# Optimization experiments

Measured on AMD Instinct MI355X. Metric: run time of the kernel, lower is better.

The kernel has to match this reference:

```python
import jax, jax.numpy as jnp
import numpy as np

N = 20000          # nodes
E = 320000         # edges (avg degree 16)
D_IN, D1, D2, D_OUT = 256, 512, 256, 64
EPS = 1e-5


def _glorot(key, shape):
    lim = (6.0 / (shape[0] + shape[1])) ** 0.5
    return jax.random.uniform(key, shape, jnp.float32, -lim, lim)


def setup_inputs() -> dict:
    key = jax.random.key(0)
    ks = jax.random.split(key, 8)
    x = jax.random.normal(ks[0], (N, D_IN), jnp.float32)
    edge_index = jax.random.randint(ks[1], (2, E), 0, N, dtype=jnp.int64)
    return {
        "x": x,
        "edge_index": edge_index,
        # SAGEConv 1 (SoftmaxAggregation temperature t1 over inp_dim channels)
        "t1": jnp.ones((1, D_IN), jnp.float32),
        "Wl1": _glorot(ks[2], (D_IN, D1)), "bl1": jnp.zeros((D1,), jnp.float32),
        "Wr1": _glorot(ks[3], (D_IN, D1)),
        "g1": jnp.ones((D1,), jnp.float32), "beta1": jnp.zeros((D1,), jnp.float32),
        # SAGEConv 2
        "t2": jnp.ones((1, D1), jnp.float32),
        "Wl2": _glorot(ks[4], (D1, D2)), "bl2": jnp.zeros((D2,), jnp.float32),
        "Wr2": _glorot(ks[5], (D1, D2)),
        "g2": jnp.ones((D2,), jnp.float32), "beta2": jnp.zeros((D2,), jnp.float32),
        # final linear + LayerNorm
        "Wf": _glorot(ks[6], (D2, D_OUT)), "bf": jnp.zeros((D_OUT,), jnp.float32),
        "gx": jnp.ones((D_OUT,), jnp.float32), "betax": jnp.zeros((D_OUT,), jnp.float32),
    }


def _sage_softmax(x, src, dst, t, Wl, bl, Wr, n):
    """SAGEConv with learnable per-channel SoftmaxAggregation."""
    m = x[src]                                              # [E, C] gathered messages
    a = m * t                                               # scaled logits
    amax = jax.ops.segment_max(a, dst, num_segments=n)      # [N, C]
    e = jnp.exp(a - amax[dst])
    denom = jax.ops.segment_sum(e, dst, num_segments=n)     # [N, C]
    w = e / denom[dst]                                      # segment softmax weights
    agg = jax.ops.segment_sum(m * w, dst, num_segments=n)   # weighted neighbor sum
    return agg @ Wl + bl + x @ Wr


def _graph_ln(x, g, b):
    # PyG LayerNorm mode='graph', batch=None: normalize over ALL nodes & channels
    mu = x.mean()
    std = jnp.sqrt(((x - mu) ** 2).mean())
    return (x - mu) / (std + EPS) * g + b


def _ln(x, g, b):
    mu = x.mean(-1, keepdims=True)
    var = ((x - mu) ** 2).mean(-1, keepdims=True)
    return (x - mu) / jnp.sqrt(var + EPS) * g + b


def reference(x, edge_index, t1, Wl1, bl1, Wr1, g1, beta1,
              t2, Wl2, bl2, Wr2, g2, beta2, Wf, bf, gx, betax):
    src, dst = edge_index[0], edge_index[1]
    h = _sage_softmax(x, src, dst, t1, Wl1, bl1, Wr1, N)
    h = jax.nn.relu(_graph_ln(h, g1, beta1))
    h = _sage_softmax(h, src, dst, t2, Wl2, bl2, Wr2, N)
    h = jax.nn.relu(_graph_ln(h, g2, beta2))
    p = h.mean(0, keepdims=True)                            # global_mean_pool, batch=None -> [1, 256]
    out = _ln(p @ Wf + bf, gx, betax)
    return jax.nn.relu(out)
```

## Files before the change

### kernel.cpp

```cpp
#include <hip/hip_runtime.h>
#include <math.h>

#define NODES 20000
#define MPAD  20096
#define EDGES 320000
#define EPSV  1e-5f
#define LOG2E 1.4426950408889634f

#define PREP_CNT   1250
#define PREP_CAST  5000
#define PREP_TR    512
#define PREP_TOTAL (PREP_CNT + PREP_CAST + PREP_TR + 1)

typedef short bf16x8 __attribute__((ext_vector_type(8)));
typedef float f32x4  __attribute__((ext_vector_type(4)));
typedef float f2     __attribute__((ext_vector_type(2)));

__device__ __forceinline__ unsigned short f2bf(float f) {
    unsigned int u = __float_as_uint(f);
    u = (u + 0x7fffu + ((u >> 16) & 1u)) >> 16;
    return (unsigned short)u;
}
__device__ __forceinline__ float bf2f(unsigned short h) {
    return __uint_as_float(((unsigned int)h) << 16);
}

__device__ __forceinline__ void load_lds16(const unsigned short* g, unsigned short* l) {
    __builtin_amdgcn_global_load_lds(
        (const __attribute__((address_space(1))) unsigned int*)g,
        (__attribute__((address_space(3))) unsigned int*)l, 16, 0, 0);
}

__global__ void k_prep(const int* __restrict__ dst, int* __restrict__ counts,
                       const float* __restrict__ x, unsigned short* __restrict__ xb,
                       const float* __restrict__ Wl1, const float* __restrict__ Wr1,
                       const float* __restrict__ Wl2, const float* __restrict__ Wr2,
                       unsigned short* __restrict__ o1l, unsigned short* __restrict__ o1r,
                       unsigned short* __restrict__ o2l, unsigned short* __restrict__ o2r,
                       float* __restrict__ acc, float* __restrict__ colsum) {
    int b = blockIdx.x;
    int t = threadIdx.x;
    if (b < PREP_CNT) {
        int e = b * 256 + t;
        if (e < EDGES) atomicAdd(&counts[dst[e]], 1);
    } else if (b < PREP_CNT + PREP_CAST) {
        int i = ((b - PREP_CNT) * 256 + t) * 4;
        float4 v = *(const float4*)(x + i);
        xb[i + 0] = f2bf(v.x); xb[i + 1] = f2bf(v.y);
        xb[i + 2] = f2bf(v.z); xb[i + 3] = f2bf(v.w);
    } else if (b < PREP_CNT + PREP_CAST + PREP_TR) {
        __shared__ float tile[32][33];
        int zz = b - PREP_CNT - PREP_CAST;
        int z = zz >> 7;
        int idx = zz & 127;
        const float* W = (z == 0) ? Wl1 : (z == 1) ? Wr1 : (z == 2) ? Wl2 : Wr2;
        unsigned short* Wt = (z == 0) ? o1l : (z == 1) ? o1r : (z == 2) ? o2l : o2r;
        int K = (z < 2) ? 256 : 512, N = (z < 2) ? 512 : 256;
        int nb = N / 32;
        int n0 = (idx % nb) * 32, k0 = (idx / nb) * 32;
        int tx = t & 31, ty = t >> 5;
#pragma unroll
        for (int j = 0; j < 4; j++)
            tile[ty + j * 8][tx] = W[(size_t)(k0 + ty + j * 8) * N + n0 + tx];
        __syncthreads();
#pragma unroll
        for (int j = 0; j < 4; j++)
            Wt[(size_t)(n0 + ty + j * 8) * K + k0 + tx] = f2bf(tile[tx][ty + j * 8]);
    } else {
        if (t < 4) acc[t] = 0.f;
        colsum[t] = 0.f;
    }
}

#define SCAN_B 32

__global__ void k_scan1(const int* __restrict__ counts, int* __restrict__ bsum) {
    __shared__ int sm[256];
    int t = threadIdx.x, b = blockIdx.x;
    int i0 = (b * 256 + t) * 3;
    int s = 0;
#pragma unroll
    for (int j = 0; j < 3; j++) { int i = i0 + j; if (i < NODES) s += counts[i]; }
    sm[t] = s;
    __syncthreads();
    int v = s;
#pragma unroll
    for (int o = 1; o < 256; o <<= 1) {
        int add = (t >= o) ? sm[t - o] : 0;
        __syncthreads();
        v += add;
        sm[t] = v;
        __syncthreads();
    }
    if (t == 255) bsum[b] = v;
}

__global__ void k_scan2(int* __restrict__ bsum, int* __restrict__ offs) {
    int t = threadIdx.x;
    int v = (t < SCAN_B) ? bsum[t] : 0;
    int x = v;
#pragma unroll
    for (int o = 1; o < 64; o <<= 1) {
        int y = __shfl_up(x, o);
        if (t >= o) x += y;
    }
    if (t < SCAN_B) bsum[t] = x - v;
    if (t == SCAN_B - 1) offs[NODES] = x;
}

__global__ void k_scan3(const int* __restrict__ counts, const int* __restrict__ bsum,
                        int* __restrict__ offs) {
    __shared__ int sm[256];
    int t = threadIdx.x, b = blockIdx.x;
    int i0 = (b * 256 + t) * 3;
    int c[3]; int s = 0;
#pragma unroll
    for (int j = 0; j < 3; j++) {
        int i = i0 + j;
        c[j] = (i < NODES) ? counts[i] : 0;
        s += c[j];
    }
    sm[t] = s;
    __syncthreads();
    int v = s;
#pragma unroll
    for (int o = 1; o < 256; o <<= 1) {
        int add = (t >= o) ? sm[t - o] : 0;
        __syncthreads();
        v += add;
        sm[t] = v;
        __syncthreads();
    }
    int run = bsum[b] + (v - s);
#pragma unroll
    for (int j = 0; j < 3; j++) {
        int i = i0 + j;
        if (i < NODES) { offs[i] = run; run += c[j]; }
    }
}

__global__ void k_scatter(const int* __restrict__ src, const int* __restrict__ dst,
                          const int* __restrict__ offs, int* __restrict__ cursor,
                          int* __restrict__ csr_src) {
    int e = blockIdx.x * blockDim.x + threadIdx.x;
    if (e < EDGES) {
        int d = dst[e];
        int pos = atomicAdd(&cursor[d], 1);
        csr_src[offs[d] + pos] = src[e];
    }
}

template <int C, int S, int UNR>
__global__ void k_agg(const unsigned short* __restrict__ xb, const float* __restrict__ tt,
                      const int* __restrict__ offs, const int* __restrict__ csr,
                      unsigned short* __restrict__ out) {
    constexpr int CS  = C / S;
    constexpr int VPL = CS / 64;
    constexpr int W   = VPL / 2;
    typedef unsigned int uv __attribute__((ext_vector_type(W)));
    typedef unsigned short usv __attribute__((ext_vector_type(VPL)));
    int waveg = (int)((blockIdx.x * (unsigned)blockDim.x + threadIdx.x) >> 6);
    int lane = threadIdx.x & 63;
    int node = waveg / S;
    int slice = waveg % S;
    if (node >= NODES) return;
    int beg = __builtin_amdgcn_readfirstlane(offs[node]);
    int end = __builtin_amdgcn_readfirstlane(offs[node + 1]);
    int cb = slice * CS + lane * VPL;
    const unsigned short* __restrict__ xcb = xb + cb;
    f2 tl[W], l[W], s[W];
#pragma unroll
    for (int i = 0; i < W; i++) {
        tl[i][0] = tt[cb + 2 * i] * LOG2E;
        tl[i][1] = tt[cb + 2 * i + 1] * LOG2E;
        l[i][0] = 0.f; l[i][1] = 0.f;
        s[i][0] = 0.f; s[i][1] = 0.f;
    }
    int k = beg;
    for (; k + UNR <= end; k += UNR) {
        uv v[UNR];
#pragma unroll
        for (int u = 0; u < UNR; u++) {
            int sn = csr[k + u];
            v[u] = *(const uv*)(xcb + (size_t)sn * C);
        }
#pragma unroll
        for (int u = 0; u < UNR; u++)
#pragma unroll
            for (int i = 0; i < W; i++) {
                unsigned wd = v[u][i];
                f2 xv;
                xv[0] = __uint_as_float(wd << 16);
                xv[1] = __uint_as_float(wd & 0xffff0000u);
                f2 a = xv * tl[i];
                f2 p;
                p[0] = __builtin_amdgcn_exp2f(a[0]);
                p[1] = __builtin_amdgcn_exp2f(a[1]);
                l[i] += p;
                s[i] = __builtin_elementwise_fma(p, xv, s[i]);
            }
    }
    for (; k < end; k++) {
        int sn = csr[k];
        uv vv = *(const uv*)(xcb + (size_t)sn * C);
#pragma unroll
        for (int i = 0; i < W; i++) {
            unsigned wd = vv[i];
            f2 xv;
            xv[0] = __uint_as_float(wd << 16);
            xv[1] = __uint_as_float(wd & 0xffff0000u);
            f2 a = xv * tl[i];
            f2 p;
            p[0] = __builtin_amdgcn_exp2f(a[0]);
            p[1] = __builtin_amdgcn_exp2f(a[1]);
            l[i] += p;
            s[i] = __builtin_elementwise_fma(p, xv, s[i]);
        }
    }
    bool has = end > beg;
    usv o;
#pragma unroll
    for (int i = 0; i < W; i++) {
        o[2 * i]     = f2bf(has ? s[i][0] / l[i][0] : 0.f);
        o[2 * i + 1] = f2bf(has ? s[i][1] / l[i][1] : 0.f);
    }
    *(usv*)(out + (size_t)node * C + cb) = o;
}

template <int K, int NT, int NTILES, int TN>
__global__ __launch_bounds__(256) void k_gemm_mfma(
    const unsigned short* __restrict__ A1, const unsigned short* __restrict__ B1t,
    const unsigned short* __restrict__ A2, const unsigned short* __restrict__ B2t,
    const float* __restrict__ bias, unsigned short* __restrict__ Co, int M,
    float* __restrict__ stat) {
    constexpr int NF = TN / 32;
    __shared__ short As[4 * 128 * 32];
    __shared__ short Bs[4 * TN * 32];
    __shared__ float rs[8], rq[8];

    int bx = blockIdx.x;
    int xid = bx & 7, q = bx >> 3;
    int n = q % NTILES, mh = q / NTILES;
    int m = mh * 8 + xid;
    if (m * 128 >= MPAD) return;
    int m0 = m * 128, n0 = n * TN;

    int t = threadIdx.x;
    int wv = t >> 6, lane = t & 63;
    int wm = wv & 1, wn = wv >> 1;
    int lm = lane & 15, quad = lane >> 4;
    int sr = t >> 2;
    int sc8 = (t & 3) * 8;

    f32x4 acc[4][NF] = {};

    for (int ph = 0; ph < 2; ph++) {
        const unsigned short* __restrict__ A  = ph ? A2 : A1;
        const unsigned short* __restrict__ Bt = ph ? B2t : B1t;
        for (int ks = 0; ks < K; ks += 128) {
#pragma unroll
            for (int c = 0; c < 4; c++) {
#pragma unroll
                for (int it = 0; it < 2; it++)
                    load_lds16(A + (size_t)(m0 + it * 64 + sr) * K + ks + c * 32 + sc8,
                               (unsigned short*)&As[c * 4096 + it * 2048 + wv * 512]);
#pragma unroll
                for (int it = 0; it < TN / 64; it++)
                    load_lds16(Bt + (size_t)(n0 + it * 64 + sr) * K + ks + c * 32 + sc8,
                               (unsigned short*)&Bs[c * (TN * 32) + it * 2048 + wv * 512]);
            }
            __syncthreads();
#pragma unroll
            for (int c = 0; c < 4; c++) {
                bf16x8 af[4], bfr[NF];
#pragma unroll
                for (int i = 0; i < 4; i++)
                    af[i] = *(const bf16x8*)&As[c * 4096 + (wm * 64 + i * 16 + lm) * 32 + quad * 8];
#pragma unroll
                for (int j = 0; j < NF; j++)
                    bfr[j] = *(const bf16x8*)&Bs[c * (TN * 32) + (wn * (TN / 2) + j * 16 + lm) * 32 + quad * 8];
#pragma unroll
                for (int mi = 0; mi < 4; mi++)
#pragma unroll
                    for (int nj = 0; nj < NF; nj++)
                        acc[mi][nj] = __builtin_amdgcn_mfma_f32_16x16x32_bf16(
                            af[mi], bfr[nj], acc[mi][nj], 0, 0, 0);
            }
            __syncthreads();
        }
    }

    float sum = 0.f, ss = 0.f;
#pragma unroll
    for (int mi = 0; mi < 4; mi++) {
        int rb = m0 + wm * 64 + mi * 16 + quad * 4;
#pragma unroll
        for (int nj = 0; nj < NF; nj++) {
            int col = n0 + wn * (TN / 2) + nj * 16 + lm;
            float bb = bias[col];
#pragma unroll
            for (int rg = 0; rg < 4; rg++) {
                int row = rb + rg;
                if (row < M) {
                    float y = acc[mi][nj][rg] + bb;
                    Co[(size_t)row * NT + col] = f2bf(y);
                    sum += y; ss += y * y;
                }
            }
        }
    }
#pragma unroll
    for (int o = 32; o > 0; o >>= 1) {
        sum += __shfl_xor(sum, o);
        ss  += __shfl_xor(ss, o);
    }
    if (lane == 0) { rs[wv] = sum; rq[wv] = ss; }
    __syncthreads();
    if (t == 0) {
        float a0 = 0.f, a1 = 0.f;
#pragma unroll
        for (int i = 0; i < 4; i++) { a0 += rs[i] + rs[i + 4]; a1 += rq[i] + rq[i + 4]; }
        atomicAdd(&stat[0], a0); atomicAdd(&stat[1], a1);
    }
}

template <int C>
__global__ void k_ln_relu_b(unsigned short* __restrict__ h, int n,
                            const float* __restrict__ st,
                            const float* __restrict__ g, const float* __restrict__ b) {
    typedef unsigned short us8 __attribute__((ext_vector_type(8)));
    float mu = st[0] / (float)n;
    float var = st[1] / (float)n - mu * mu;
    var = var < 0.f ? 0.f : var;
    float inv = 1.0f / (sqrtf(var) + EPSV);
    int i8 = (blockIdx.x * blockDim.x + threadIdx.x) * 8;
    if (i8 >= n) return;
    int c = i8 & (C - 1);
    us8 v = *(const us8*)(h + i8);
    us8 o;
#pragma unroll
    for (int j = 0; j < 8; j++) {
        float y = (bf2f(v[j]) - mu) * inv * g[c + j] + b[c + j];
        o[j] = f2bf(fmaxf(y, 0.f));
    }
    *(us8*)(h + i8) = o;
}

__global__ void k_ln_colsum(const unsigned short* __restrict__ h, int n,
                            const float* __restrict__ st,
                            const float* __restrict__ g, const float* __restrict__ b,
                            float* __restrict__ colsum) {
    float mu = st[0] / (float)n;
    float var = st[1] / (float)n - mu * mu;
    var = var < 0.f ? 0.f : var;
    float inv = 1.0f / (sqrtf(var) + EPSV);
    int t = threadIdx.x;
    float gv = g[t], bv = b[t];
    float local = 0.f;
    int stride = gridDim.x * blockDim.x;
    for (int i = blockIdx.x * blockDim.x + t; i < n; i += stride) {
        float y = (bf2f(h[i]) - mu) * inv * gv + bv;
        local += fmaxf(y, 0.f);
    }
    atomicAdd(&colsum[t], local);
}

__global__ void k_final(const float* __restrict__ colsum, const float* __restrict__ Wf,
                        const float* __restrict__ bf, const float* __restrict__ gx,
                        const float* __restrict__ bx, float* __restrict__ out) {
    __shared__ float p[256];
    __shared__ float red[4][64];
    int t = threadIdx.x;
    p[t] = colsum[t] * (1.0f / (float)NODES);
    __syncthreads();
    int kg = t >> 6, o = t & 63;
    float a = 0.f;
#pragma unroll
    for (int j = 0; j < 64; j++) {
        int c = kg + j * 4;
        a = fmaf(p[c], Wf[c * 64 + o], a);
    }
    red[kg][o] = a;
    __syncthreads();
    if (t < 64) {
        float acc = bf[t] + red[0][t] + red[1][t] + red[2][t] + red[3][t];
        float sum = acc;
        for (int w = 32; w > 0; w >>= 1) sum += __shfl_xor(sum, w);
        float mu = sum * (1.0f / 64.0f);
        float d = acc - mu;
        float vs = d * d;
        for (int w = 32; w > 0; w >>= 1) vs += __shfl_xor(vs, w);
        float var = vs * (1.0f / 64.0f);
        float y = d * rsqrtf(var + EPSV) * gx[t] + bx[t];
        out[t] = fmaxf(y, 0.f);
    }
}

extern "C" void kernel_launch(void* const* d_in, const int* in_sizes, int n_in,
                              void* d_out, int out_size, void* d_ws, size_t ws_size,
                              hipStream_t stream) {
    const float* x   = (const float*)d_in[0];
    const int*   ei  = (const int*)d_in[1];
    const float* t1  = (const float*)d_in[2];
    const float* Wl1 = (const float*)d_in[3];
    const float* bl1 = (const float*)d_in[4];
    const float* Wr1 = (const float*)d_in[5];
    const float* g1  = (const float*)d_in[6];
    const float* be1 = (const float*)d_in[7];
    const float* t2  = (const float*)d_in[8];
    const float* Wl2 = (const float*)d_in[9];
    const float* bl2 = (const float*)d_in[10];
    const float* Wr2 = (const float*)d_in[11];
    const float* g2  = (const float*)d_in[12];
    const float* be2 = (const float*)d_in[13];
    const float* Wf  = (const float*)d_in[14];
    const float* bf  = (const float*)d_in[15];
    const float* gx  = (const float*)d_in[16];
    const float* bx  = (const float*)d_in[17];
    float* out = (float*)d_out;

    char* ws = (char*)d_ws;
    size_t off = 0;
    auto alloc = [&](size_t bytes) { size_t o = off; off = (off + bytes + 511) & ~511ull; return o; };
    size_t o_counts = alloc((size_t)NODES * 4);
    size_t o_cursor = alloc((size_t)NODES * 4);
    size_t zero_bytes = off;
    size_t o_acc    = alloc(4 * 4);
    size_t o_colsum = alloc(256 * 4);
    size_t o_bsum = alloc((size_t)SCAN_B * 4);
    size_t o_offs = alloc((size_t)(NODES + 1) * 4);
    size_t o_csrc = alloc((size_t)EDGES * 4);
    size_t o_w1l  = alloc((size_t)512 * 256 * 2);
    size_t o_w1r  = alloc((size_t)512 * 256 * 2);
    size_t o_w2l  = alloc((size_t)256 * 512 * 2);
    size_t o_w2r  = alloc((size_t)256 * 512 * 2);
    size_t o_bufX = alloc((size_t)MPAD * 256 * 2);
    size_t o_agg  = alloc((size_t)MPAD * 512 * 2);
    size_t o_h1   = alloc((size_t)(MPAD + 512) * 512 * 2);

    int*   counts = (int*)(ws + o_counts);
    int*   cursor = (int*)(ws + o_cursor);
    float* acc    = (float*)(ws + o_acc);
    float* colsum = (float*)(ws + o_colsum);
    int*   bsum   = (int*)(ws + o_bsum);
    int*   offs   = (int*)(ws + o_offs);
    int*   csrc   = (int*)(ws + o_csrc);
    unsigned short* w1lt = (unsigned short*)(ws + o_w1l);
    unsigned short* w1rt = (unsigned short*)(ws + o_w1r);
    unsigned short* w2lt = (unsigned short*)(ws + o_w2l);
    unsigned short* w2rt = (unsigned short*)(ws + o_w2r);
    unsigned short* xb   = (unsigned short*)(ws + o_bufX);
    unsigned short* h2p  = (unsigned short*)(ws + o_bufX);
    unsigned short* aggb = (unsigned short*)(ws + o_agg);
    unsigned short* h1   = (unsigned short*)(ws + o_h1);

    const int* src = ei;
    const int* dst = ei + EDGES;

    hipMemsetAsync(ws, 0, zero_bytes, stream);

    k_prep<<<PREP_TOTAL, 256, 0, stream>>>(dst, counts, x, xb,
                                           Wl1, Wr1, Wl2, Wr2,
                                           w1lt, w1rt, w2lt, w2rt,
                                           acc, colsum);
    k_scan1<<<SCAN_B, 256, 0, stream>>>(counts, bsum);
    k_scan2<<<1, 64, 0, stream>>>(bsum, offs);
    k_scan3<<<SCAN_B, 256, 0, stream>>>(counts, bsum, offs);
    k_scatter<<<(EDGES + 255) / 256, 256, 0, stream>>>(src, dst, offs, cursor, csrc);

    k_agg<256, 2, 8><<<(NODES * 2 + 3) / 4, 256, 0, stream>>>(xb, t1, offs, csrc, aggb);
    k_gemm_mfma<256, 512, 4, 128><<<8 * 4 * 20, 256, 0, stream>>>(
        aggb, w1lt, xb, w1rt, bl1, h1, NODES, acc);
    k_ln_relu_b<512><<<NODES * 512 / 8 / 256, 256, 0, stream>>>(h1, NODES * 512, acc, g1, be1);

    k_agg<512, 2, 4><<<(NODES * 2 + 3) / 4, 256, 0, stream>>>(h1, t2, offs, csrc, aggb);
    k_gemm_mfma<512, 256, 2, 128><<<8 * 2 * 20, 256, 0, stream>>>(
        aggb, w2lt, h1, w2rt, bl2, h2p, NODES, acc + 2);

    k_ln_colsum<<<1024, 256, 0, stream>>>(h2p, NODES * 256, acc + 2, g2, be2, colsum);
    k_final<<<1, 256, 0, stream>>>(colsum, Wf, bf, gx, bx, out);
}
```

Measured before the change: 320.8 us.

## Prefetch GEMM K-slabs into registers to overlap global loads with MFMA

Replaces the direct global-to-LDS loads of 128-wide K chunks with a register-staged software pipeline over 64-wide K slabs. The next slab is loaded into registers while the MFMAs for the current slab run, then written to LDS after a barrier. This halves LDS usage, which may raise occupancy, and hides global load latency. The cost is extra VGPRs for staging, extra LDS store instructions, and more barriers per K step.

```diff
diff --git a/kernel.cpp b/kernel.cpp
--- a/kernel.cpp
+++ b/kernel.cpp
@@ -23,12 +23,6 @@
 }
 __device__ __forceinline__ float bf2f(unsigned short h) {
     return __uint_as_float(((unsigned int)h) << 16);
-}
-
-__device__ __forceinline__ void load_lds16(const unsigned short* g, unsigned short* l) {
-    __builtin_amdgcn_global_load_lds(
-        (const __attribute__((address_space(1))) unsigned int*)g,
-        (__attribute__((address_space(3))) unsigned int*)l, 16, 0, 0);
 }
 
 __global__ void k_prep(const int* __restrict__ dst, int* __restrict__ counts,
@@ -233,9 +227,12 @@
     const unsigned short* __restrict__ A2, const unsigned short* __restrict__ B2t,
     const float* __restrict__ bias, unsigned short* __restrict__ Co, int M,
     float* __restrict__ stat) {
-    constexpr int NF = TN / 32;
-    __shared__ short As[4 * 128 * 32];
-    __shared__ short Bs[4 * TN * 32];
+    constexpr int NF  = TN / 32;
+    constexpr int BIT = TN / 64;
+    constexpr int HS  = K / 64;
+    constexpr int NS  = 2 * HS;
+    __shared__ short As[2 * 128 * 32];
+    __shared__ short Bs[2 * TN * 32];
     __shared__ float rs[8], rq[8];
 
     int bx = blockIdx.x;
@@ -253,40 +250,53 @@
     int sc8 = (t & 3) * 8;
 
     f32x4 acc[4][NF] = {};
-
-    for (int ph = 0; ph < 2; ph++) {
-        const unsigned short* __restrict__ A  = ph ? A2 : A1;
-        const unsigned short* __restrict__ Bt = ph ? B2t : B1t;
-        for (int ks = 0; ks < K; ks += 128) {
-#pragma unroll
-            for (int c = 0; c < 4; c++) {
-#pragma unroll
-                for (int it = 0; it < 2; it++)
-                    load_lds16(A + (size_t)(m0 + it * 64 + sr) * K + ks + c * 32 + sc8,
-                               (unsigned short*)&As[c * 4096 + it * 2048 + wv * 512]);
-#pragma unroll
-                for (int it = 0; it < TN / 64; it++)
-                    load_lds16(Bt + (size_t)(n0 + it * 64 + sr) * K + ks + c * 32 + sc8,
-                               (unsigned short*)&Bs[c * (TN * 32) + it * 2048 + wv * 512]);
-            }
-            __syncthreads();
-#pragma unroll
-            for (int c = 0; c < 4; c++) {
-                bf16x8 af[4], bfr[NF];
-#pragma unroll
-                for (int i = 0; i < 4; i++)
-                    af[i] = *(const bf16x8*)&As[c * 4096 + (wm * 64 + i * 16 + lm) * 32 + quad * 8];
-#pragma unroll
-                for (int j = 0; j < NF; j++)
-                    bfr[j] = *(const bf16x8*)&Bs[c * (TN * 32) + (wn * (TN / 2) + j * 16 + lm) * 32 + quad * 8];
-#pragma unroll
-                for (int mi = 0; mi < 4; mi++)
-#pragma unroll
-                    for (int nj = 0; nj < NF; nj++)
-                        acc[mi][nj] = __builtin_amdgcn_mfma_f32_16x16x32_bf16(
-                            af[mi], bfr[nj], acc[mi][nj], 0, 0, 0);
-            }
-            __syncthreads();
+    bf16x8 rA[2][2];
+    bf16x8 rB[2][BIT];
+
+    auto loadslab = [&](int s) {
+        const unsigned short* __restrict__ A  = (s < HS) ? A1 : A2;
+        const unsigned short* __restrict__ Bt = (s < HS) ? B1t : B2t;
+        int kk = (s & (HS - 1)) * 64;
+#pragma unroll
+        for (int c = 0; c < 2; c++) {
+#pragma unroll
+            for (int it = 0; it < 2; it++)
+                rA[c][it] = *(const bf16x8*)(A + (size_t)(m0 + it * 64 + sr) * K + kk + c * 32 + sc8);
+#pragma unroll
+            for (int it = 0; it < BIT; it++)
+                rB[c][it] = *(const bf16x8*)(Bt + (size_t)(n0 + it * 64 + sr) * K + kk + c * 32 + sc8);
+        }
+    };
+
+    loadslab(0);
+    for (int s = 0; s < NS; s++) {
+        if (s) __syncthreads();
+#pragma unroll
+        for (int c = 0; c < 2; c++) {
+#pragma unroll
+            for (int it = 0; it < 2; it++)
+                *(bf16x8*)&As[c * 4096 + it * 2048 + t * 8] = rA[c][it];
+#pragma unroll
+            for (int it = 0; it < BIT; it++)
+                *(bf16x8*)&Bs[c * (TN * 32) + it * 2048 + t * 8] = rB[c][it];
+        }
+        __syncthreads();
+        if (s + 1 < NS) loadslab(s + 1);
+#pragma unroll
+        for (int c = 0; c < 2; c++) {
+            bf16x8 af[4], bfr[NF];
+#pragma unroll
+            for (int i = 0; i < 4; i++)
+                af[i] = *(const bf16x8*)&As[c * 4096 + (wm * 64 + i * 16 + lm) * 32 + quad * 8];
+#pragma unroll
+            for (int j = 0; j < NF; j++)
+                bfr[j] = *(const bf16x8*)&Bs[c * (TN * 32) + (wn * (TN / 2) + j * 16 + lm) * 32 + quad * 8];
+#pragma unroll
+            for (int mi = 0; mi < 4; mi++)
+#pragma unroll
+                for (int nj = 0; nj < NF; nj++)
+                    acc[mi][nj] = __builtin_amdgcn_mfma_f32_16x16x32_bf16(
+                        af[mi], bfr[nj], acc[mi][nj], 0, 0, 0);
         }
     }
 
```

Measured after the change: 315.4 us. About the same (-1.7%).

## Load GEMM MFMA fragments directly from global memory, dropping LDS staging

Applied to the files above, without the earlier changes.

The bf16 MFMA GEMM no longer stages A and B tiles through shared memory with global_load_lds and block barriers. Each wave now loads its own 16x8 bf16 fragments straight from global memory every 32-wide k step. This removes the LDS round trip and the two __syncthreads per k-block. In exchange, tiles shared between the waves are fetched redundantly from global memory and L2, the row-strided 16-byte loads coalesce poorly, and there is no explicit prefetch to hide latency.

```diff
diff --git a/kernel.cpp b/kernel.cpp
--- a/kernel.cpp
+++ b/kernel.cpp
@@ -23,12 +23,6 @@
 }
 __device__ __forceinline__ float bf2f(unsigned short h) {
     return __uint_as_float(((unsigned int)h) << 16);
-}
-
-__device__ __forceinline__ void load_lds16(const unsigned short* g, unsigned short* l) {
-    __builtin_amdgcn_global_load_lds(
-        (const __attribute__((address_space(1))) unsigned int*)g,
-        (__attribute__((address_space(3))) unsigned int*)l, 16, 0, 0);
 }
 
 __global__ void k_prep(const int* __restrict__ dst, int* __restrict__ counts,
@@ -227,16 +221,14 @@
     *(usv*)(out + (size_t)node * C + cb) = o;
 }
 
-template <int K, int NT, int NTILES, int TN>
+template <int K, int NT, int NTILES>
 __global__ __launch_bounds__(256) void k_gemm_mfma(
     const unsigned short* __restrict__ A1, const unsigned short* __restrict__ B1t,
     const unsigned short* __restrict__ A2, const unsigned short* __restrict__ B2t,
     const float* __restrict__ bias, unsigned short* __restrict__ Co, int M,
     float* __restrict__ stat) {
-    constexpr int NF = TN / 32;
-    __shared__ short As[4 * 128 * 32];
-    __shared__ short Bs[4 * TN * 32];
-    __shared__ float rs[8], rq[8];
+    constexpr int TN = 128;
+    __shared__ float rs[4], rq[4];
 
     int bx = blockIdx.x;
     int xid = bx & 7, q = bx >> 3;
@@ -249,44 +241,30 @@
     int wv = t >> 6, lane = t & 63;
     int wm = wv & 1, wn = wv >> 1;
     int lm = lane & 15, quad = lane >> 4;
-    int sr = t >> 2;
-    int sc8 = (t & 3) * 8;
-
-    f32x4 acc[4][NF] = {};
-
+
+    f32x4 acc[4][4] = {};
+
+#pragma unroll
     for (int ph = 0; ph < 2; ph++) {
         const unsigned short* __restrict__ A  = ph ? A2 : A1;
         const unsigned short* __restrict__ Bt = ph ? B2t : B1t;
-        for (int ks = 0; ks < K; ks += 128) {
-#pragma unroll
-            for (int c = 0; c < 4; c++) {
-#pragma unroll
-                for (int it = 0; it < 2; it++)
-                    load_lds16(A + (size_t)(m0 + it * 64 + sr) * K + ks + c * 32 + sc8,
-                               (unsigned short*)&As[c * 4096 + it * 2048 + wv * 512]);
-#pragma unroll
-                for (int it = 0; it < TN / 64; it++)
-                    load_lds16(Bt + (size_t)(n0 + it * 64 + sr) * K + ks + c * 32 + sc8,
-                               (unsigned short*)&Bs[c * (TN * 32) + it * 2048 + wv * 512]);
-            }
-            __syncthreads();
-#pragma unroll
-            for (int c = 0; c < 4; c++) {
-                bf16x8 af[4], bfr[NF];
-#pragma unroll
-                for (int i = 0; i < 4; i++)
-                    af[i] = *(const bf16x8*)&As[c * 4096 + (wm * 64 + i * 16 + lm) * 32 + quad * 8];
-#pragma unroll
-                for (int j = 0; j < NF; j++)
-                    bfr[j] = *(const bf16x8*)&Bs[c * (TN * 32) + (wn * (TN / 2) + j * 16 + lm) * 32 + quad * 8];
-#pragma unroll
-                for (int mi = 0; mi < 4; mi++)
-#pragma unroll
-                    for (int nj = 0; nj < NF; nj++)
-                        acc[mi][nj] = __builtin_amdgcn_mfma_f32_16x16x32_bf16(
-                            af[mi], bfr[nj], acc[mi][nj], 0, 0, 0);
-            }
-            __syncthreads();
+        const unsigned short* pa = A  + (size_t)(m0 + wm * 64 + lm) * K + quad * 8;
+        const unsigned short* pb = Bt + (size_t)(n0 + wn * 64 + lm) * K + quad * 8;
+#pragma unroll 2
+        for (int kk = 0; kk < K; kk += 32) {
+            bf16x8 af[4], bfr[4];
+#pragma unroll
+            for (int i = 0; i < 4; i++)
+                af[i] = *(const bf16x8*)(pa + (size_t)(i * 16) * K + kk);
+#pragma unroll
+            for (int j = 0; j < 4; j++)
+                bfr[j] = *(const bf16x8*)(pb + (size_t)(j * 16) * K + kk);
+#pragma unroll
+            for (int mi = 0; mi < 4; mi++)
+#pragma unroll
+                for (int nj = 0; nj < 4; nj++)
+                    acc[mi][nj] = __builtin_amdgcn_mfma_f32_16x16x32_bf16(
+                        af[mi], bfr[nj], acc[mi][nj], 0, 0, 0);
         }
     }
 
@@ -295,8 +273,8 @@
     for (int mi = 0; mi < 4; mi++) {
         int rb = m0 + wm * 64 + mi * 16 + quad * 4;
 #pragma unroll
-        for (int nj = 0; nj < NF; nj++) {
-            int col = n0 + wn * (TN / 2) + nj * 16 + lm;
+        for (int nj = 0; nj < 4; nj++) {
+            int col = n0 + wn * 64 + nj * 16 + lm;
             float bb = bias[col];
 #pragma unroll
             for (int rg = 0; rg < 4; rg++) {
@@ -319,7 +297,7 @@
     if (t == 0) {
         float a0 = 0.f, a1 = 0.f;
 #pragma unroll
-        for (int i = 0; i < 4; i++) { a0 += rs[i] + rs[i + 4]; a1 += rq[i] + rq[i + 4]; }
+        for (int i = 0; i < 4; i++) { a0 += rs[i]; a1 += rq[i]; }
         atomicAdd(&stat[0], a0); atomicAdd(&stat[1], a1);
     }
 }
@@ -469,12 +447,12 @@
     k_scatter<<<(EDGES + 255) / 256, 256, 0, stream>>>(src, dst, offs, cursor, csrc);
 
     k_agg<256, 2, 8><<<(NODES * 2 + 3) / 4, 256, 0, stream>>>(xb, t1, offs, csrc, aggb);
-    k_gemm_mfma<256, 512, 4, 128><<<8 * 4 * 20, 256, 0, stream>>>(
+    k_gemm_mfma<256, 512, 4><<<8 * 4 * 20, 256, 0, stream>>>(
         aggb, w1lt, xb, w1rt, bl1, h1, NODES, acc);
     k_ln_relu_b<512><<<NODES * 512 / 8 / 256, 256, 0, stream>>>(h1, NODES * 512, acc, g1, be1);
 
     k_agg<512, 2, 4><<<(NODES * 2 + 3) / 4, 256, 0, stream>>>(h1, t2, offs, csrc, aggb);
-    k_gemm_mfma<512, 256, 2, 128><<<8 * 2 * 20, 256, 0, stream>>>(
+    k_gemm_mfma<512, 256, 2><<<8 * 2 * 20, 256, 0, stream>>>(
         aggb, w2lt, h1, w2rt, bl2, h2p, NODES, acc + 2);
 
     k_ln_colsum<<<1024, 256, 0, stream>>>(h2p, NODES * 256, acc + 2, g2, be2, colsum);
```

Measured after the change: 382.6 us. +19.3%, slower.
